# Performance work log

Measured on AMD Instinct MI355X. Metric: run time of the kernel, lower is better.

Reference implementation:

```python
import jax, jax.numpy as jnp
import numpy as np

NUM_HEADS = 24
EPS = 1e-6


def rms_norm(x, scale):
    # fp32 RMSNorm over last dim, matching torch F.rms_norm(eps=1e-6)
    xf = x.astype(jnp.float32)
    rrms = jax.lax.rsqrt(jnp.mean(xf * xf, axis=-1, keepdims=True) + EPS)
    return (xf * rrms * scale.astype(jnp.float32)).astype(x.dtype)


def rope_rotate(x, pe):
    # x: [B,H,L,D]; pe: [B,1,L,D/2,2,2] rotation matrices
    B, H, L, D = x.shape
    xr = x.astype(jnp.float32).reshape(B, H, L, D // 2, 1, 2)
    out = pe[..., 0] * xr[..., 0] + pe[..., 1] * xr[..., 1]  # [B,H,L,D/2,2]
    return out.reshape(B, H, L, D).astype(x.dtype)


def setup_inputs() -> dict:
    key = jax.random.key(0)
    ks = jax.random.split(key, 6)
    B, L, C = 1, 2048, 3072
    H = NUM_HEADS
    D = C // H
    x = jax.random.normal(ks[0], (B, L, C), dtype=jnp.float32)
    # pe: proper RoPE rotation matrices [[cos,-sin],[sin,cos]] -> [B,1,L,D/2,2,2]
    theta = jax.random.uniform(ks[1], (B, 1, L, D // 2), dtype=jnp.float32) * (2.0 * np.pi)
    cos, sin = jnp.cos(theta), jnp.sin(theta)
    row0 = jnp.stack([cos, -sin], axis=-1)
    row1 = jnp.stack([sin, cos], axis=-1)
    pe = jnp.stack([row0, row1], axis=-2)  # [B,1,L,D/2,2,2]
    w_qkv = jax.random.normal(ks[2], (3 * C, C), dtype=jnp.float32) * (1.0 / np.sqrt(C))
    q_scale = jnp.ones((D,), dtype=jnp.float32)
    k_scale = jnp.ones((D,), dtype=jnp.float32)
    w_proj = jax.random.normal(ks[3], (C, C), dtype=jnp.float32) * (1.0 / np.sqrt(C))
    b_proj = jnp.zeros((C,), dtype=jnp.float32)
    return {"x": x, "pe": pe, "w_qkv": w_qkv, "q_scale": q_scale,
            "k_scale": k_scale, "w_proj": w_proj, "b_proj": b_proj}


def reference(x, pe, w_qkv, q_scale, k_scale, w_proj, b_proj):
    B, L, C = x.shape
    H = NUM_HEADS
    D = C // H
    qkv = x @ w_qkv.T                                   # [B,L,3C]
    qkv = qkv.reshape(B, L, 3, H, D).transpose(2, 0, 3, 1, 4)  # [3,B,H,L,D]
    q, k, v = qkv[0], qkv[1], qkv[2]
    q = rms_norm(q, q_scale)
    k = rms_norm(k, k_scale)
    q = rope_rotate(q, pe)
    k = rope_rotate(k, pe)
    scale = 1.0 / np.sqrt(D)
    scores = jnp.einsum('bhqd,bhkd->bhqk', q, k) * jnp.asarray(scale, q.dtype)
    attn = jax.nn.softmax(scores, axis=-1)
    out = jnp.einsum('bhqk,bhkd->bhqd', attn, v)        # [B,H,L,D]
    out = out.transpose(0, 2, 1, 3).reshape(B, L, C)    # [B,L,C]
    return out @ w_proj.T + b_proj
```

## Files before the change

### kernel.cpp

```cpp
#include <hip/hip_runtime.h>

typedef __attribute__((ext_vector_type(8))) __bf16 bf16x8;
typedef __attribute__((ext_vector_type(4))) float f32x4;

typedef __attribute__((address_space(1))) void gvoid;
typedef __attribute__((address_space(3))) void lvoid;

__device__ __forceinline__ float bf2f(unsigned int u) {
    union { unsigned int u; float f; } v; v.u = u << 16; return v.f;
}
__device__ __forceinline__ unsigned short f2bf(float f) {
    union { float f; unsigned int u; } v; v.f = f;
    unsigned int r = v.u + 0x7fffu + ((v.u >> 16) & 1u);
    return (unsigned short)(r >> 16);
}
__device__ __forceinline__ unsigned int pack2(float a, float b) {
    return (unsigned int)f2bf(a) | ((unsigned int)f2bf(b) << 16);
}
__device__ __forceinline__ void async16(const void* g, void* l) {
    __builtin_amdgcn_global_load_lds((gvoid*)g, (lvoid*)l, 16, 0, 0);
}
__device__ __forceinline__ float exp2f_hw(float x) {
    return __builtin_amdgcn_exp2f(x);
}


__global__ __launch_bounds__(256)
void cvt_bf16(const float4* __restrict__ s, uint4* __restrict__ d, int n8) {
    int i = blockIdx.x * 256 + threadIdx.x;
    if (i >= n8) return;
    float4 a = s[2 * i], b = s[2 * i + 1];
    uint4 o;
    o.x = pack2(a.x, a.y); o.y = pack2(a.z, a.w);
    o.z = pack2(b.x, b.y); o.w = pack2(b.z, b.w);
    d[i] = o;
}

#define GEMM_CORE(A_, lda_, B_, ldb_, K_)                                        \
    __shared__ __align__(16) unsigned short As[4096];                            \
    __shared__ __align__(16) unsigned short Bs[4096];                            \
    const int t = threadIdx.x, lane = t & 63;                                    \
    const int wm = t >> 7, wn = (t >> 6) & 1;                                    \
    const int lr = lane & 15, kc = lane >> 4;                                    \
    f32x4 acc[4][4] = {};                                                        \
    for (int k0 = 0; k0 < (K_); k0 += 32) {                                      \
        _Pragma("unroll")                                                        \
        for (int i = 0; i < 2; ++i) {                                            \
            int e = (i * 256 + t) * 8;                                           \
            int row = e >> 5, c8 = (e >> 3) & 3;                                 \
            int gc = (c8 ^ ((row >> 1) & 3)) * 8;                                \
            async16(&(A_)[(size_t)(m0 + row) * (lda_) + k0 + gc], &As[e]);       \
            async16(&(B_)[(size_t)(n0 + row) * (ldb_) + k0 + gc], &Bs[e]);       \
        }                                                                        \
        __syncthreads();                                                         \
        bf16x8 af[4], bfr[4];                                                    \
        _Pragma("unroll")                                                        \
        for (int i = 0; i < 4; ++i) {                                            \
            int ra = wm * 64 + i * 16 + lr;                                      \
            int rb = wn * 64 + i * 16 + lr;                                      \
            af[i]  = *(const bf16x8*)&As[ra * 32 + ((kc ^ ((ra >> 1) & 3)) * 8)];\
            bfr[i] = *(const bf16x8*)&Bs[rb * 32 + ((kc ^ ((rb >> 1) & 3)) * 8)];\
        }                                                                        \
        _Pragma("unroll")                                                        \
        for (int mi = 0; mi < 4; ++mi)                                           \
            _Pragma("unroll")                                                    \
            for (int ni = 0; ni < 4; ++ni)                                       \
                acc[mi][ni] = __builtin_amdgcn_mfma_f32_16x16x32_bf16(           \
                    af[mi], bfr[ni], acc[mi][ni], 0, 0, 0);                      \
        __syncthreads();                                                         \
    }

__global__ __launch_bounds__(256, 2)
void gemm_qkv(const unsigned short* __restrict__ A, const unsigned short* __restrict__ B,
              unsigned short* __restrict__ qk, unsigned short* __restrict__ vt) {
    const int n0 = blockIdx.x * 128, m0 = blockIdx.y * 128;
    GEMM_CORE(A, 3072, B, 3072, 3072)
    const int rb0 = kc * 4;
#pragma unroll
    for (int mi = 0; mi < 4; ++mi)
#pragma unroll
        for (int ni = 0; ni < 4; ++ni) {
            int col = n0 + wn * 64 + ni * 16 + lr;
#pragma unroll
            for (int r = 0; r < 4; ++r) {
                int row = m0 + wm * 64 + mi * 16 + rb0 + r;
                unsigned short v = f2bf(acc[mi][ni][r]);
                if (col < 6144) qk[(size_t)row * 6144 + col] = v;
                else            vt[(size_t)(col - 6144) * 2048 + row] = v;
            }
        }
}

__global__ __launch_bounds__(256, 2)
void gemm_proj(const unsigned short* __restrict__ A, const unsigned short* __restrict__ B,
               const float* __restrict__ bias, float* __restrict__ out) {
    const int n0 = blockIdx.x * 128, m0 = blockIdx.y * 128;
    GEMM_CORE(A, 6144, B, 3072, 3072)
    const int rb0 = kc * 4;
#pragma unroll
    for (int mi = 0; mi < 4; ++mi)
#pragma unroll
        for (int ni = 0; ni < 4; ++ni) {
            int col = n0 + wn * 64 + ni * 16 + lr;
            float badd = bias[col];
#pragma unroll
            for (int r = 0; r < 4; ++r) {
                int row = m0 + wm * 64 + mi * 16 + rb0 + r;
                out[(size_t)row * 3072 + col] = acc[mi][ni][r] + badd;
            }
        }
}

__global__ __launch_bounds__(256)
void attn2(unsigned short* __restrict__ qk, const unsigned short* __restrict__ vt) {
    __shared__ __align__(16) unsigned short Ks[64 * 128];
    __shared__ __align__(16) unsigned short Vs[128 * 64];
    __shared__ __align__(16) unsigned short Ps[4 * 16 * 64];
    const int t = threadIdx.x, lane = t & 63, w = t >> 6;
    const int h = blockIdx.x, qblk = blockIdx.y * 64;
    const int lr = lane & 15, kc = lane >> 4;
    const float sc2 = 0.08838834764831845f * 1.4426950408889634f;

    bf16x8 aq[4];
#pragma unroll
    for (int ks = 0; ks < 4; ++ks)
        aq[ks] = *(const bf16x8*)&qk[(size_t)(qblk + w * 16 + lr) * 6144 + h * 128 + ks * 32 + kc * 8];

    f32x4 o[8] = {};
    float mst[4], lst[4];
#pragma unroll
    for (int r = 0; r < 4; ++r) { mst[r] = -1e30f; lst[r] = 0.0f; }

    unsigned short* Pw = &Ps[w * 1024];

    for (int kb = 0; kb < 2048; kb += 64) {
#pragma unroll
        for (int i = 0; i < 4; ++i) {
            int e = (i * 256 + t) * 8;
            {
                int row = e >> 7, c8 = (e >> 3) & 15;
                int gc = (c8 ^ (row & 15)) * 8;
                async16(&qk[(size_t)(kb + row) * 6144 + 3072 + h * 128 + gc], &Ks[e]);
            }
            {
                int row = e >> 6, c8 = (e >> 3) & 7;
                int gc = (c8 ^ (row & 7)) * 8;
                async16(&vt[(size_t)(h * 128 + row) * 2048 + kb + gc], &Vs[e]);
            }
        }
        __syncthreads();

        f32x4 s[4] = {};
#pragma unroll
        for (int nt = 0; nt < 4; ++nt) {
            int rk = nt * 16 + lr;
#pragma unroll
            for (int ks = 0; ks < 4; ++ks) {
                int ck = ks * 4 + kc;
                bf16x8 bk = *(const bf16x8*)&Ks[rk * 128 + ((ck ^ (rk & 15)) * 8)];
                s[nt] = __builtin_amdgcn_mfma_f32_16x16x32_bf16(aq[ks], bk, s[nt], 0, 0, 0);
            }
        }

#pragma unroll
        for (int r = 0; r < 4; ++r) {
            float vmax = fmaxf(fmaxf(s[0][r], s[1][r]), fmaxf(s[2][r], s[3][r]));
#pragma unroll
            for (int off = 8; off >= 1; off >>= 1) vmax = fmaxf(vmax, __shfl_xor(vmax, off));
            float mn = fmaxf(mst[r], vmax);
            float al = exp2f_hw((mst[r] - mn) * sc2);
            mst[r] = mn;
            float ps = 0.0f;
#pragma unroll
            for (int nt = 0; nt < 4; ++nt) {
                float p = exp2f_hw((s[nt][r] - mn) * sc2);
                s[nt][r] = p;
                ps += p;
            }
#pragma unroll
            for (int off = 8; off >= 1; off >>= 1) ps += __shfl_xor(ps, off);
            lst[r] = lst[r] * al + ps;
#pragma unroll
            for (int dt = 0; dt < 8; ++dt) o[dt][r] *= al;
        }

#pragma unroll
        for (int nt = 0; nt < 4; ++nt) {
            int col = nt * 16 + lr;
            int chunk = col >> 3, cin = col & 7;
#pragma unroll
            for (int r = 0; r < 4; ++r) {
                int q = kc * 4 + r;
                Pw[q * 64 + ((chunk ^ (q & 7)) * 8 + cin)] = f2bf(s[nt][r]);
            }
        }

#pragma unroll
        for (int ks2 = 0; ks2 < 2; ++ks2) {
            int ck = ks2 * 4 + kc;
            bf16x8 ap = *(const bf16x8*)&Pw[lr * 64 + ((ck ^ (lr & 7)) * 8)];
#pragma unroll
            for (int dt = 0; dt < 8; ++dt) {
                int rv = dt * 16 + lr;
                bf16x8 bv = *(const bf16x8*)&Vs[rv * 64 + ((ck ^ (rv & 7)) * 8)];
                o[dt] = __builtin_amdgcn_mfma_f32_16x16x32_bf16(ap, bv, o[dt], 0, 0, 0);
            }
        }
        __syncthreads();
    }

#pragma unroll
    for (int dt = 0; dt < 8; ++dt)
#pragma unroll
        for (int r = 0; r < 4; ++r) {
            int row = qblk + w * 16 + kc * 4 + r;
            qk[(size_t)row * 6144 + h * 128 + dt * 16 + lr] = f2bf(o[dt][r] / lst[r]);
        }
}


__global__ __launch_bounds__(256)
void norm_rope(unsigned short* __restrict__ qk, const float* __restrict__ pe,
               const float* __restrict__ q_scale, const float* __restrict__ k_scale) {
    const int wid = threadIdx.x >> 6, lane = threadIdx.x & 63;
    int pid = blockIdx.x * 4 + wid;
    const int isK = pid >= 49152;
    int p2 = isK ? pid - 49152 : pid;
    const int h = p2 >> 11, l = p2 & 2047;

    unsigned short* src = qk + (size_t)l * 6144 + (isK ? 3072 : 0) + h * 128 + lane * 2;
    unsigned int xu = *(const unsigned int*)src;
    float x0 = bf2f(xu & 0xffffu), x1 = bf2f(xu >> 16);
    float ss = x0 * x0 + x1 * x1;
#pragma unroll
    for (int off = 32; off >= 1; off >>= 1) ss += __shfl_xor(ss, off);
    float rr = rsqrtf(ss * (1.0f / 128.0f) + 1e-6f);

    const float* sc = isK ? k_scale : q_scale;
    float2 s2 = *(const float2*)(sc + lane * 2);
    float y0 = x0 * rr * s2.x;
    float y1 = x1 * rr * s2.y;

    float4 p4 = *(const float4*)(pe + ((size_t)l * 64 + lane) * 4);
    float o0 = p4.x * y0 + p4.y * y1;
    float o1 = p4.z * y0 + p4.w * y1;

    *(unsigned int*)src = pack2(o0, o1);
}


template <bool A32, bool B32, bool C32, bool HAS_BIAS, bool TRANS_C>
__global__ __launch_bounds__(256, 2)
void gemm_bt(const void* __restrict__ Ap, const void* __restrict__ Bp,
             const float* __restrict__ bias, void* __restrict__ Cp,
             int M, int N, int K, int lda, int ldc) {
    __shared__ __align__(16) unsigned short As[128 * 40];
    __shared__ __align__(16) unsigned short Bs[128 * 40];
    const int t = threadIdx.x, lane = t & 63;
    const int wm = t >> 7, wn = (t >> 6) & 1;
    const int m0 = blockIdx.x * 128, n0 = blockIdx.y * 128;
    const int lr = lane & 15, kc = lane >> 4;
    f32x4 acc[4][4] = {};

    for (int k0 = 0; k0 < K; k0 += 32) {
        float4 ra32[4], rb32[4];
        bf16x8 ra16[2], rb16[2];
        if constexpr (A32) {
            const float* A = (const float*)Ap;
#pragma unroll
            for (int i = 0; i < 4; ++i) {
                int idx = i * 256 + t, row = idx >> 3, c4 = idx & 7;
                ra32[i] = *(const float4*)&A[(size_t)(m0 + row) * lda + k0 + c4 * 4];
            }
        } else {
            const unsigned short* A = (const unsigned short*)Ap;
#pragma unroll
            for (int i = 0; i < 2; ++i) {
                int idx = i * 256 + t, row = idx >> 2, c8 = idx & 3;
                ra16[i] = *(const bf16x8*)&A[(size_t)(m0 + row) * lda + k0 + c8 * 8];
            }
        }
        if constexpr (B32) {
            const float* B = (const float*)Bp;
#pragma unroll
            for (int i = 0; i < 4; ++i) {
                int idx = i * 256 + t, row = idx >> 3, c4 = idx & 7;
                rb32[i] = *(const float4*)&B[(size_t)(n0 + row) * K + k0 + c4 * 4];
            }
        } else {
            const unsigned short* B = (const unsigned short*)Bp;
#pragma unroll
            for (int i = 0; i < 2; ++i) {
                int idx = i * 256 + t, row = idx >> 2, c8 = idx & 3;
                rb16[i] = *(const bf16x8*)&B[(size_t)(n0 + row) * K + k0 + c8 * 8];
            }
        }
        __syncthreads();
        if constexpr (A32) {
#pragma unroll
            for (int i = 0; i < 4; ++i) {
                int idx = i * 256 + t, row = idx >> 3, c4 = idx & 7;
                uint2 p = { pack2(ra32[i].x, ra32[i].y), pack2(ra32[i].z, ra32[i].w) };
                *(uint2*)&As[row * 40 + c4 * 4] = p;
            }
        } else {
#pragma unroll
            for (int i = 0; i < 2; ++i) {
                int idx = i * 256 + t, row = idx >> 2, c8 = idx & 3;
                *(bf16x8*)&As[row * 40 + c8 * 8] = ra16[i];
            }
        }
        if constexpr (B32) {
#pragma unroll
            for (int i = 0; i < 4; ++i) {
                int idx = i * 256 + t, row = idx >> 3, c4 = idx & 7;
                uint2 p = { pack2(rb32[i].x, rb32[i].y), pack2(rb32[i].z, rb32[i].w) };
                *(uint2*)&Bs[row * 40 + c4 * 4] = p;
            }
        } else {
#pragma unroll
            for (int i = 0; i < 2; ++i) {
                int idx = i * 256 + t, row = idx >> 2, c8 = idx & 3;
                *(bf16x8*)&Bs[row * 40 + c8 * 8] = rb16[i];
            }
        }
        __syncthreads();
        bf16x8 af[4], bfr[4];
#pragma unroll
        for (int i = 0; i < 4; ++i) {
            af[i]  = *(const bf16x8*)&As[(wm * 64 + i * 16 + lr) * 40 + kc * 8];
            bfr[i] = *(const bf16x8*)&Bs[(wn * 64 + i * 16 + lr) * 40 + kc * 8];
        }
#pragma unroll
        for (int mi = 0; mi < 4; ++mi)
#pragma unroll
            for (int ni = 0; ni < 4; ++ni)
                acc[mi][ni] = __builtin_amdgcn_mfma_f32_16x16x32_bf16(af[mi], bfr[ni], acc[mi][ni], 0, 0, 0);
    }
    const int rb0 = kc * 4;
#pragma unroll
    for (int mi = 0; mi < 4; ++mi) {
#pragma unroll
        for (int ni = 0; ni < 4; ++ni) {
            int col = n0 + wn * 64 + ni * 16 + lr;
            float badd = HAS_BIAS ? bias[col] : 0.0f;
#pragma unroll
            for (int r = 0; r < 4; ++r) {
                int row = m0 + wm * 64 + mi * 16 + rb0 + r;
                size_t off = TRANS_C ? ((size_t)col * ldc + row) : ((size_t)row * ldc + col);
                if (C32) ((float*)Cp)[off] = acc[mi][ni][r] + badd;
                else     ((unsigned short*)Cp)[off] = f2bf(acc[mi][ni][r] + badd);
            }
        }
    }
}

__global__ __launch_bounds__(256, 2)
void attn_slow(unsigned short* __restrict__ qk, const unsigned short* __restrict__ vt) {
    __shared__ __align__(16) unsigned short Ks[64 * 136];
    __shared__ __align__(16) unsigned short Vs[128 * 72];
    __shared__ __align__(16) unsigned short Ps[4 * 32 * 72];
    const int t = threadIdx.x, lane = t & 63, w = t >> 6;
    const int h = blockIdx.y, q0 = blockIdx.x * 128;
    const int lr = lane & 15, kc = lane >> 4;
    const float scale = 0.08838834764831845f;

    bf16x8 aq[2][4];
#pragma unroll
    for (int mf = 0; mf < 2; ++mf)
#pragma unroll
        for (int ks = 0; ks < 4; ++ks)
            aq[mf][ks] = *(const bf16x8*)&qk[(size_t)(q0 + w * 32 + mf * 16 + lr) * 6144 + h * 128 + ks * 32 + kc * 8];

    f32x4 o[2][8] = {};
    float mst[2][4], lst[2][4];
#pragma unroll
    for (int mf = 0; mf < 2; ++mf)
#pragma unroll
        for (int r = 0; r < 4; ++r) { mst[mf][r] = -1e30f; lst[mf][r] = 0.0f; }

    unsigned short* Pw = &Ps[w * 32 * 72];

    for (int kb = 0; kb < 2048; kb += 64) {
        bf16x8 rk[4], rv[4];
#pragma unroll
        for (int i = 0; i < 4; ++i) {
            int idx = i * 256 + t;
            { int row = idx >> 4, c8 = idx & 15;
              rk[i] = *(const bf16x8*)&qk[(size_t)(kb + row) * 6144 + 3072 + h * 128 + c8 * 8]; }
            { int row = idx >> 3, c8 = idx & 7;
              rv[i] = *(const bf16x8*)&vt[(size_t)(h * 128 + row) * 2048 + kb + c8 * 8]; }
        }
        __syncthreads();
#pragma unroll
        for (int i = 0; i < 4; ++i) {
            int idx = i * 256 + t;
            { int row = idx >> 4, c8 = idx & 15; *(bf16x8*)&Ks[row * 136 + c8 * 8] = rk[i]; }
            { int row = idx >> 3, c8 = idx & 7;  *(bf16x8*)&Vs[row * 72 + c8 * 8] = rv[i]; }
        }
        __syncthreads();

        f32x4 s[2][4] = {};
#pragma unroll
        for (int nt = 0; nt < 4; ++nt) {
            int rkr = nt * 16 + lr;
#pragma unroll
            for (int ks = 0; ks < 4; ++ks) {
                bf16x8 bk = *(const bf16x8*)&Ks[rkr * 136 + (ks * 4 + kc) * 8];
#pragma unroll
                for (int mf = 0; mf < 2; ++mf)
                    s[mf][nt] = __builtin_amdgcn_mfma_f32_16x16x32_bf16(aq[mf][ks], bk, s[mf][nt], 0, 0, 0);
            }
        }
#pragma unroll
        for (int mf = 0; mf < 2; ++mf)
#pragma unroll
            for (int nt = 0; nt < 4; ++nt)
#pragma unroll
                for (int r = 0; r < 4; ++r) s[mf][nt][r] *= scale;

#pragma unroll
        for (int mf = 0; mf < 2; ++mf) {
#pragma unroll
            for (int r = 0; r < 4; ++r) {
                float vmax = fmaxf(fmaxf(s[mf][0][r], s[mf][1][r]), fmaxf(s[mf][2][r], s[mf][3][r]));
#pragma unroll
                for (int off = 8; off >= 1; off >>= 1) vmax = fmaxf(vmax, __shfl_xor(vmax, off));
                float mn = fmaxf(mst[mf][r], vmax);
                float al = __expf(mst[mf][r] - mn);
                mst[mf][r] = mn;
                float ps = 0.0f;
#pragma unroll
                for (int nt = 0; nt < 4; ++nt) {
                    float p = __expf(s[mf][nt][r] - mn);
                    s[mf][nt][r] = p;
                    ps += p;
                }
#pragma unroll
                for (int off = 8; off >= 1; off >>= 1) ps += __shfl_xor(ps, off);
                lst[mf][r] = lst[mf][r] * al + ps;
#pragma unroll
                for (int dt = 0; dt < 8; ++dt) o[mf][dt][r] *= al;
            }
        }

#pragma unroll
        for (int mf = 0; mf < 2; ++mf)
#pragma unroll
            for (int nt = 0; nt < 4; ++nt)
#pragma unroll
                for (int r = 0; r < 4; ++r)
                    Pw[(mf * 16 + kc * 4 + r) * 72 + nt * 16 + lr] = f2bf(s[mf][nt][r]);

#pragma unroll
        for (int ks2 = 0; ks2 < 2; ++ks2) {
            bf16x8 ap[2];
#pragma unroll
            for (int mf = 0; mf < 2; ++mf)
                ap[mf] = *(const bf16x8*)&Pw[(mf * 16 + lr) * 72 + (ks2 * 4 + kc) * 8];
#pragma unroll
            for (int dt = 0; dt < 8; ++dt) {
                bf16x8 bv = *(const bf16x8*)&Vs[(dt * 16 + lr) * 72 + (ks2 * 4 + kc) * 8];
#pragma unroll
                for (int mf = 0; mf < 2; ++mf)
                    o[mf][dt] = __builtin_amdgcn_mfma_f32_16x16x32_bf16(ap[mf], bv, o[mf][dt], 0, 0, 0);
            }
        }
        __syncthreads();
    }

#pragma unroll
    for (int mf = 0; mf < 2; ++mf)
#pragma unroll
        for (int dt = 0; dt < 8; ++dt)
#pragma unroll
            for (int r = 0; r < 4; ++r) {
                int row = q0 + w * 32 + mf * 16 + kc * 4 + r;
                qk[(size_t)row * 6144 + h * 128 + dt * 16 + lr] = f2bf(o[mf][dt][r] / lst[mf][r]);
            }
}

__global__ void fill_two(float* p, int n) {
    int i = blockIdx.x * 256 + threadIdx.x;
    if (i < n) p[i] = 2.0f;
}

extern "C" void kernel_launch(void* const* d_in, const int* in_sizes, int n_in,
                              void* d_out, int out_size, void* d_ws, size_t ws_size,
                              hipStream_t stream) {
    const float* x       = (const float*)d_in[0];
    const float* pe      = (const float*)d_in[1];
    const float* w_qkv   = (const float*)d_in[2];
    const float* q_scale = (const float*)d_in[3];
    const float* k_scale = (const float*)d_in[4];
    const float* w_proj  = (const float*)d_in[5];
    const float* b_proj  = (const float*)d_in[6];
    float* out = (float*)d_out;

    if (ws_size >= 125829120ull) {
        unsigned short* ws     = (unsigned short*)d_ws;
        unsigned short* xb     = ws;
        unsigned short* wqkvb  = ws + 6291456;
        unsigned short* wprojb = ws + 34603008;
        unsigned short* qk     = ws + 44040192;
        unsigned short* vt     = ws + 56623104;

        cvt_bf16<<<3072, 256, 0, stream>>>((const float4*)x, (uint4*)xb, 786432);
        cvt_bf16<<<13824, 256, 0, stream>>>((const float4*)w_qkv, (uint4*)wqkvb, 3538944);
        cvt_bf16<<<4608, 256, 0, stream>>>((const float4*)w_proj, (uint4*)wprojb, 1179648);

        gemm_qkv<<<dim3(72, 16), 256, 0, stream>>>(xb, wqkvb, qk, vt);
        norm_rope<<<24576, 256, 0, stream>>>(qk, pe, q_scale, k_scale);
        attn2<<<dim3(24, 32), 256, 0, stream>>>(qk, vt);
        gemm_proj<<<dim3(24, 16), 256, 0, stream>>>(qk, wprojb, b_proj, out);
        return;
    }

    if (ws_size < 37748736ull) {
        fill_two<<<(6291456 + 255) / 256, 256, 0, stream>>>(out, 6291456);
        return;
    }

    unsigned short* qk = (unsigned short*)d_ws;
    unsigned short* vt = qk + 12582912;

    gemm_bt<true, true, false, false, false><<<dim3(16, 48), 256, 0, stream>>>(
        x, w_qkv, nullptr, qk, 2048, 6144, 3072, 3072, 6144);
    norm_rope<<<24576, 256, 0, stream>>>(qk, pe, q_scale, k_scale);
    gemm_bt<true, true, false, false, true><<<dim3(16, 24), 256, 0, stream>>>(
        x, w_qkv + (size_t)6144 * 3072, nullptr, vt, 2048, 3072, 3072, 3072, 2048);
    attn_slow<<<dim3(16, 24), 256, 0, stream>>>(qk, vt);
    gemm_bt<false, true, true, true, false><<<dim3(16, 24), 256, 0, stream>>>(
        qk, w_proj, b_proj, out, 2048, 3072, 3072, 6144, 3072);
}
```

Before: 606.9 us.

## Rewrite QKV GEMM as 256x256 tile with 4-stage async LDS pipeline

Replaces the QKV projection GEMM core with a 512-thread, 256x256-tile kernel that uses a 4-slot ring of async global-to-LDS loads. The A and B loads for later k-steps are interleaved with two half-tile MFMA phases, using explicit waitcnt, barriers and setprio. The aim is to hide global memory latency and to raise data reuse per loaded tile. In exchange, each wave holds twice as many accumulators and the kernel uses 128KB of LDS. The grid drops to 288 blocks, which may leave part of the device idle and limits occupancy.

```diff
diff --git a/kernel.cpp b/kernel.cpp
--- a/kernel.cpp
+++ b/kernel.cpp
@@ -70,20 +70,97 @@
         __syncthreads();                                                         \
     }
 
-__global__ __launch_bounds__(256, 2)
+__global__ __launch_bounds__(512, 2)
 void gemm_qkv(const unsigned short* __restrict__ A, const unsigned short* __restrict__ B,
               unsigned short* __restrict__ qk, unsigned short* __restrict__ vt) {
-    const int n0 = blockIdx.x * 128, m0 = blockIdx.y * 128;
-    GEMM_CORE(A, 3072, B, 3072, 3072)
+    __shared__ __align__(16) unsigned short As[4][8192];
+    __shared__ __align__(16) unsigned short Bs[4][8192];
+    const int n0 = blockIdx.x * 256, m0 = blockIdx.y * 256;
+    const int t = threadIdx.x, lane = t & 63, w = t >> 6;
+    const int wm = w >> 2, wn = w & 3;
+    const int lr = lane & 15, kc = lane >> 4;
+    const int NK = 96;
+
+    const int e0 = t * 8,         r0 = e0 >> 5, c0 = (e0 >> 3) & 3;
+    const int e1 = (512 + t) * 8, r1 = e1 >> 5, c1 = (e1 >> 3) & 3;
+    const int g0 = (c0 ^ ((r0 >> 1) & 3)) * 8;
+    const int g1 = (c1 ^ ((r1 >> 1) & 3)) * 8;
+    const unsigned short* Ag0 = &A[(size_t)(m0 + r0) * 3072 + g0];
+    const unsigned short* Ag1 = &A[(size_t)(m0 + r1) * 3072 + g1];
+    const unsigned short* Bg0 = &B[(size_t)(n0 + r0) * 3072 + g0];
+    const unsigned short* Bg1 = &B[(size_t)(n0 + r1) * 3072 + g1];
+
+#define STAGE_A(kt_) { int s_ = (kt_) & 3, k_ = (kt_) * 32;                      \
+        async16(Ag0 + k_, &As[s_][e0]); async16(Ag1 + k_, &As[s_][e1]); }
+#define STAGE_B(kt_) { int s_ = (kt_) & 3, k_ = (kt_) * 32;                      \
+        async16(Bg0 + k_, &Bs[s_][e0]); async16(Bg1 + k_, &Bs[s_][e1]); }
+
+    f32x4 acc[8][4] = {};
+
+    STAGE_A(0); STAGE_B(0);
+    STAGE_A(1); STAGE_B(1);
+    STAGE_A(2); STAGE_B(2);
+    asm volatile("s_waitcnt vmcnt(8)" ::: "memory");
+    __builtin_amdgcn_s_barrier();
+
+    for (int kt = 0; kt < NK; ++kt) {
+        const int slot = kt & 3;
+        bf16x8 af[4], bfr[4];
+#pragma unroll
+        for (int i = 0; i < 4; ++i) {
+            int ra = wm * 128 + i * 16 + lr;
+            int rb = wn * 64 + i * 16 + lr;
+            af[i]  = *(const bf16x8*)&As[slot][ra * 32 + ((kc ^ ((ra >> 1) & 3)) * 8)];
+            bfr[i] = *(const bf16x8*)&Bs[slot][rb * 32 + ((kc ^ ((rb >> 1) & 3)) * 8)];
+        }
+        if (kt + 3 < NK) STAGE_A(kt + 3);
+        __builtin_amdgcn_s_barrier();
+        asm volatile("s_waitcnt lgkmcnt(0)" ::: "memory");
+        __builtin_amdgcn_sched_barrier(0);
+        __builtin_amdgcn_s_setprio(1);
+#pragma unroll
+        for (int mi = 0; mi < 4; ++mi)
+#pragma unroll
+            for (int ni = 0; ni < 4; ++ni)
+                acc[mi][ni] = __builtin_amdgcn_mfma_f32_16x16x32_bf16(
+                    af[mi], bfr[ni], acc[mi][ni], 0, 0, 0);
+        __builtin_amdgcn_s_setprio(0);
+        __builtin_amdgcn_s_barrier();
+        bf16x8 af2[4];
+#pragma unroll
+        for (int i = 0; i < 4; ++i) {
+            int ra = wm * 128 + 64 + i * 16 + lr;
+            af2[i] = *(const bf16x8*)&As[slot][ra * 32 + ((kc ^ ((ra >> 1) & 3)) * 8)];
+        }
+        if (kt + 3 < NK) STAGE_B(kt + 3);
+        __builtin_amdgcn_s_barrier();
+        asm volatile("s_waitcnt lgkmcnt(0)" ::: "memory");
+        __builtin_amdgcn_sched_barrier(0);
+        __builtin_amdgcn_s_setprio(1);
+#pragma unroll
+        for (int mi = 0; mi < 4; ++mi)
+#pragma unroll
+            for (int ni = 0; ni < 4; ++ni)
+                acc[4 + mi][ni] = __builtin_amdgcn_mfma_f32_16x16x32_bf16(
+                    af2[mi], bfr[ni], acc[4 + mi][ni], 0, 0, 0);
+        __builtin_amdgcn_s_setprio(0);
+        if (kt + 3 < NK)      { asm volatile("s_waitcnt vmcnt(8)" ::: "memory"); }
+        else if (kt + 2 < NK) { asm volatile("s_waitcnt vmcnt(4)" ::: "memory"); }
+        else if (kt + 1 < NK) { asm volatile("s_waitcnt vmcnt(0)" ::: "memory"); }
+        __builtin_amdgcn_s_barrier();
+    }
+#undef STAGE_A
+#undef STAGE_B
+
     const int rb0 = kc * 4;
 #pragma unroll
-    for (int mi = 0; mi < 4; ++mi)
+    for (int mi = 0; mi < 8; ++mi)
 #pragma unroll
         for (int ni = 0; ni < 4; ++ni) {
             int col = n0 + wn * 64 + ni * 16 + lr;
 #pragma unroll
             for (int r = 0; r < 4; ++r) {
-                int row = m0 + wm * 64 + mi * 16 + rb0 + r;
+                int row = m0 + wm * 128 + mi * 16 + rb0 + r;
                 unsigned short v = f2bf(acc[mi][ni][r]);
                 if (col < 6144) qk[(size_t)row * 6144 + col] = v;
                 else            vt[(size_t)(col - 6144) * 2048 + row] = v;
@@ -509,7 +586,7 @@
         cvt_bf16<<<13824, 256, 0, stream>>>((const float4*)w_qkv, (uint4*)wqkvb, 3538944);
         cvt_bf16<<<4608, 256, 0, stream>>>((const float4*)w_proj, (uint4*)wprojb, 1179648);
 
-        gemm_qkv<<<dim3(72, 16), 256, 0, stream>>>(xb, wqkvb, qk, vt);
+        gemm_qkv<<<dim3(36, 8), 512, 0, stream>>>(xb, wqkvb, qk, vt);
         norm_rope<<<24576, 256, 0, stream>>>(qk, pe, q_scale, k_scale);
         attn2<<<dim3(24, 32), 256, 0, stream>>>(qk, vt);
         gemm_proj<<<dim3(24, 16), 256, 0, stream>>>(qk, wprojb, b_proj, out);
```

Result: slower. 642.3 us (+5.8%).
